# Kernel optimization log

Hardware: AMD Instinct MI355X
Metric: run time of the kernel (lower is better)

Reference implementation:

```python
import jax, jax.numpy as jnp
import numpy as np

B = 256
IN_CH = 1
E = 8          # embedding_channels (power of 2)
DEPTH = 3      # log2(E)
T = 8192       # time_range
WINDOW = 2.0
K = 15         # kernel_size (odd -> torch 'same' == lax 'SAME')
TPI = 2.0 * np.pi


def conv1d(x, w, b, dilation=1, groups=1):
    # x: (B, Cin, T), w: (Cout, Cin/groups, K), b: (Cout,)
    out = jax.lax.conv_general_dilated(
        x, w, window_strides=(1,), padding='SAME',
        rhs_dilation=(dilation,),
        dimension_numbers=('NCH', 'OIH', 'NCH'),
        feature_group_count=groups)
    return out + b[None, :, None]


def setup_inputs() -> dict:
    key = jax.random.key(0)
    ks = jax.random.split(key, 14)
    s = 0.05
    x = jax.random.normal(ks[0], (B, T), jnp.float32)
    W1 = jax.random.normal(ks[1], (E, 2, 1, K), jnp.float32) * s   # per-channel Conv1d(1,2)
    b1 = jax.random.normal(ks[2], (E, 2), jnp.float32) * s
    W2 = jax.random.normal(ks[3], (E, 1, 2, K), jnp.float32) * s   # per-channel Conv1d(2,1)
    b2 = jax.random.normal(ks[4], (E, 1), jnp.float32) * s
    fcW = jax.random.normal(ks[5], (E, 2, T), jnp.float32) * 0.01  # per-channel Linear(T, 2)
    fcb = jax.random.normal(ks[6], (E, 2), jnp.float32) * s
    # deconv tree: level j has 2**(DEPTH-1-j) Conv1d(2,1) units, stacked as grouped conv
    dW0 = jax.random.normal(ks[7], (4, 2, K), jnp.float32) * s
    db0 = jax.random.normal(ks[8], (4,), jnp.float32) * s
    dW1 = jax.random.normal(ks[9], (2, 2, K), jnp.float32) * s
    db1 = jax.random.normal(ks[10], (2,), jnp.float32) * s
    dW2 = jax.random.normal(ks[11], (1, 2, K), jnp.float32) * s
    db2 = jax.random.normal(ks[12], (1,), jnp.float32) * s
    return dict(x=x, W1=W1, b1=b1, W2=W2, b2=b2, fcW=fcW, fcb=fcb,
                dW0=dW0, db0=db0, dW1=dW1, db1=db1, dW2=dW2, db2=db2)


def reference(x, W1, b1, W2, b2, fcW, fcb, dW0, db0, dW1, db1, dW2, db2):
    y = x.reshape(x.shape[0], IN_CH, T)
    # per-channel dilated conv stack (dilation = 2**i)
    chans = []
    for i in range(E):
        h = conv1d(y, W1[i], b1[i], dilation=2 ** i)
        chans.append(conv1d(h, W2[i], b2[i], dilation=2 ** i))
    latent = jnp.concatenate(chans, axis=1)                # (B, E, T)
    # FFT -> frequency / amplitude / offset
    rfft = jnp.fft.rfft(latent, axis=2)                    # (B, E, T//2+1)
    power = jnp.abs(rfft[:, :, 1:]) ** 2
    freqs = jnp.asarray(np.fft.rfftfreq(T)[1:] * T / WINDOW, jnp.float32)
    psum = jnp.sum(power, axis=2)
    f = jnp.sum(freqs * power, axis=2) / psum              # (B, E)
    a = 2.0 * jnp.sqrt(psum) / T
    b_off = rfft.real[:, :, 0] / T
    # per-channel Linear(T, 2) -> phase
    v = jnp.einsum('bet,ect->bec', latent, fcW) + fcb      # (B, E, 2)
    p = jnp.arctan2(v[..., 1], v[..., 0]) / TPI            # (B, E)
    # sinusoid reconstruction
    args = jnp.linspace(-WINDOW / 2, WINDOW / 2, T, dtype=jnp.float32)
    sig = a[..., None] * jnp.sin(TPI * (f[..., None] * args + p[..., None])) + b_off[..., None]
    # deconv tree: pairs of channels -> grouped conv, halving channels each level
    y = sig
    for dW, db in ((dW0, db0), (dW1, db1), (dW2, db2)):
        y = conv1d(y, dW, db, dilation=1, groups=dW.shape[0])
    out = y.reshape(y.shape[0], IN_CH * T)
    return (out, latent, sig,
            p[..., None], f[..., None], a[..., None], b_off[..., None])
```

## Files before the change

kernel.cpp:

```cpp
#include <hip/hip_runtime.h>
#include <math.h>

#define TT 8192
#define BB 256
#define EE 8
#define KK 15
#define PI_F  3.14159265358979323846f
#define TPI_F 6.28318530717958647692f

#define OFF_OUT 0
#define OFF_LAT (BB*TT)
#define OFF_SIG (OFF_LAT + BB*EE*TT)
#define OFF_P   (OFF_SIG + BB*EE*TT)
#define OFF_F   (OFF_P + BB*EE)
#define OFF_A   (OFF_F + BB*EE)
#define OFF_B0  (OFF_A + BB*EE)

#define TILE_C 1024

#define SWZ(i) ((i) + ((i) >> 5))

__global__ __launch_bounds__(512) void conv_stack_kernel(
    const float* __restrict__ x, const float* __restrict__ W1,
    const float* __restrict__ b1, const float* __restrict__ W2,
    const float* __restrict__ b2, float* __restrict__ latent)
{
  extern __shared__ float smem[];
  const int e = blockIdx.x, b = blockIdx.y;
  const int d  = 1 << e;
  const int M  = TT >> e;
  const int Lp = ((((M - 2) + 31) >> 5) << 5) + 30;
  float* sxp = smem;
  float* sW  = smem + d * Lp;
  const int tid = threadIdx.x;
  const float* xr = x + b * TT;

  const int nstage = TT + 28 * d;
  for (int i = tid; i < nstage; i += 512) {
    int t  = i - 14 * d;
    int ph = i & (d - 1);
    int n  = i >> e;
    sxp[ph * Lp + n] = (t >= 0 && t < TT) ? xr[t] : 0.0f;
  }

  if (tid < 29) {
    float acc = 0.0f;
    for (int c = 0; c < 2; c++) {
      const float* w1 = W1 + e*30 + c*15;
      const float* w2 = W2 + e*30 + c*15;
      int jlo = tid - 14; if (jlo < 0) jlo = 0;
      int jhi = tid;      if (jhi > 14) jhi = 14;
      for (int j = jlo; j <= jhi; j++) acc += w2[j] * w1[tid - j];
    }
    sW[tid] = acc;
  } else if (tid == 29) {
    float s20 = 0.f, s21 = 0.f;
    for (int j = 0; j < 15; j++) { s20 += W2[e*30 + j]; s21 += W2[e*30 + 15 + j]; }
    sW[29] = b2[e] + s20*b1[e*2] + s21*b1[e*2 + 1];
  } else if (tid >= 32 && tid < 62) {
    sW[tid] = W1[e*30 + (tid - 32)];
  } else if (tid >= 64 && tid < 94) {
    sW[tid] = W2[e*30 + (tid - 64)];
  } else if (tid == 94 || tid == 95) {
    sW[tid] = b1[e*2 + (tid - 94)];
  }
  __syncthreads();

  float W[29];
  #pragma unroll
  for (int s = 0; s < 29; s++) W[s] = sW[s];
  const float Bc = sW[29];

  float* lr = latent + (b * EE + e) * TT;
  #pragma unroll 1
  for (int g = 0; g < 4; g++) {
    const int vt = g * 512 + tid;
    const int ph = vt & (d - 1);
    const int m0 = (vt >> e) << 2;
    const int row = ph * Lp;

    float win[32];
    {
      const float2* wp = (const float2*)&sxp[row + m0];
      #pragma unroll
      for (int v = 0; v < 16; v++) {
        float2 qv = wp[v];
        win[2*v] = qv.x; win[2*v+1] = qv.y;
      }
    }
    float acc[4] = {Bc, Bc, Bc, Bc};
    #pragma unroll
    for (int s = 0; s < 29; s++) {
      #pragma unroll
      for (int r = 0; r < 4; r++) acc[r] = fmaf(W[s], win[s + r], acc[r]);
    }

    if (g == 0 && m0 <= 6) {
      float h0[10], h1[10];
      #pragma unroll
      for (int s = 0; s < 10; s++) {
        float a0 = sW[94], a1 = sW[95];
        #pragma unroll
        for (int k = 0; k < 15; k++) {
          float xv = win[s + k];
          a0 = fmaf(sW[32 + k], xv, a0);
          a1 = fmaf(sW[47 + k], xv, a1);
        }
        h0[s] = a0; h1[s] = a1;
      }
      #pragma unroll
      for (int r = 0; r < 4; r++) {
        float corr = 0.0f;
        #pragma unroll
        for (int j = 0; j < 7; j++) {
          if (m0 + r + j <= 6) {
            corr = fmaf(sW[64 + j], h0[r + j], corr);
            corr = fmaf(sW[79 + j], h1[r + j], corr);
          }
        }
        acc[r] -= corr;
      }
    }
    if (g == 3 && m0 + 3 >= M - 7) {
      float h0[10], h1[10];
      #pragma unroll
      for (int s = 0; s < 10; s++) {
        float a0 = sW[94], a1 = sW[95];
        #pragma unroll
        for (int k = 0; k < 15; k++) {
          float xv = win[8 + s + k];
          a0 = fmaf(sW[32 + k], xv, a0);
          a1 = fmaf(sW[47 + k], xv, a1);
        }
        h0[s] = a0; h1[s] = a1;
      }
      #pragma unroll
      for (int r = 0; r < 4; r++) {
        float corr = 0.0f;
        #pragma unroll
        for (int jj = 0; jj < 7; jj++) {
          const int j = 8 + jj;
          if (m0 + r + j >= M + 7) {
            corr = fmaf(sW[64 + j], h0[r + jj], corr);
            corr = fmaf(sW[79 + j], h1[r + jj], corr);
          }
        }
        acc[r] -= corr;
      }
    }

    #pragma unroll
    for (int r = 0; r < 4; r++) lr[ph + (m0 + r) * d] = acc[r];
  }
}

#define NF 4096

__device__ __forceinline__ int rev4(int k) {
  unsigned r = __brev((unsigned)k) >> 20;
  return (int)(((r & 0x555u) << 1) | ((r >> 1) & 0x555u));
}

__global__ __launch_bounds__(512) void fft_kernel(
    const float* __restrict__ latent, const float* __restrict__ fcW,
    const float* __restrict__ fcb, float* __restrict__ outP,
    float* __restrict__ outF, float* __restrict__ outA, float* __restrict__ outB0)
{
  __shared__ float re[SWZ(NF - 1) + 1];
  __shared__ float im[SWZ(NF - 1) + 1];
  __shared__ float rbuf[32];
  const int e = blockIdx.x, b = blockIdx.y, tid = threadIdx.x;
  const float2* row2 = (const float2*)(latent + (b*EE + e)*TT);
  const float2* f02  = (const float2*)(fcW + (e*2 + 0)*TT);
  const float2* f12  = (const float2*)(fcW + (e*2 + 1)*TT);

  float v0 = 0.f, v1 = 0.f;
  for (int n = tid; n < NF; n += 512) {
    float2 z = row2[n];
    re[SWZ(n)] = z.x; im[SWZ(n)] = z.y;
    float2 a0 = f02[n], a1 = f12[n];
    v0 = fmaf(z.x, a0.x, v0); v0 = fmaf(z.y, a0.y, v0);
    v1 = fmaf(z.x, a1.x, v1); v1 = fmaf(z.y, a1.y, v1);
  }
  __syncthreads();

  for (int L = NF >> 2; L >= 1; L >>= 2) {
    float wstep = -1.57079632679f / (float)L;
    for (int u = tid; u < (NF >> 2); u += 512) {
      int p = u & (L - 1);
      int base = ((u - p) << 2) + p;
      int i0 = SWZ(base), i1 = SWZ(base + L), i2 = SWZ(base + 2*L), i3 = SWZ(base + 3*L);
      float ar = re[i0], ai = im[i0];
      float br = re[i1], bi = im[i1];
      float cr = re[i2], ci = im[i2];
      float dr = re[i3], di = im[i3];
      float t0r = ar + cr, t0i = ai + ci;
      float t1r = ar - cr, t1i = ai - ci;
      float t2r = br + dr, t2i = bi + di;
      float t3r = br - dr, t3i = bi - di;
      float A0r = t0r + t2r, A0i = t0i + t2i;
      float A1r = t1r + t3i, A1i = t1i - t3r;
      float A2r = t0r - t2r, A2i = t0i - t2i;
      float A3r = t1r - t3i, A3i = t1i + t3r;
      float ang = wstep * (float)p;
      float s1 = __sinf(ang), c1 = __cosf(ang);
      float c2 = c1*c1 - s1*s1, s2 = 2.f*c1*s1;
      float c3 = c1*c2 - s1*s2, s3 = c1*s2 + s1*c2;
      re[i0] = A0r;                 im[i0] = A0i;
      re[i1] = A1r*c1 - A1i*s1;     im[i1] = A1r*s1 + A1i*c1;
      re[i2] = A2r*c2 - A2i*s2;     im[i2] = A2r*s2 + A2i*c2;
      re[i3] = A3r*c3 - A3i*s3;     im[i3] = A3r*s3 + A3i*c3;
    }
    __syncthreads();
  }

  float pacc = 0.f, facc = 0.f;
  for (int k = 1 + tid; k < NF; k += 512) {
    int jk = SWZ(rev4(k));
    int jm = SWZ(rev4(NF - k));
    float zr = re[jk], zi = im[jk];
    float yr = re[jm], yi = im[jm];
    float Er = 0.5f*(zr + yr), Ei = 0.5f*(zi - yi);
    float Dr = 0.5f*(zr - yr), Di = 0.5f*(zi + yi);
    float Or = Di, Oi = -Dr;
    float ang = -PI_F * (float)k / (float)NF;
    float s = __sinf(ang), c = __cosf(ang);
    float Xr = Er + c*Or - s*Oi;
    float Xi = Ei + c*Oi + s*Or;
    float mag = fmaf(Xr, Xr, Xi*Xi);
    pacc += mag;
    facc = fmaf(0.5f * (float)k, mag, facc);
  }
  if (tid == 0) {
    float X = re[SWZ(0)] - im[SWZ(0)];
    pacc += X*X;
    facc += 2048.0f * X*X;
  }

  #pragma unroll
  for (int off = 32; off > 0; off >>= 1) {
    pacc += __shfl_down(pacc, off);
    facc += __shfl_down(facc, off);
    v0   += __shfl_down(v0, off);
    v1   += __shfl_down(v1, off);
  }
  int wid = tid >> 6, lane = tid & 63;
  if (lane == 0) {
    rbuf[wid*4 + 0] = pacc; rbuf[wid*4 + 1] = facc;
    rbuf[wid*4 + 2] = v0;   rbuf[wid*4 + 3] = v1;
  }
  __syncthreads();
  if (tid == 0) {
    float P = 0.f, Fw = 0.f, V0 = 0.f, V1 = 0.f;
    #pragma unroll
    for (int w = 0; w < 8; w++) {
      P += rbuf[w*4]; Fw += rbuf[w*4+1]; V0 += rbuf[w*4+2]; V1 += rbuf[w*4+3];
    }
    float z0r = re[SWZ(0)], z0i = im[SWZ(0)];
    float amp  = 2.0f * sqrtf(P) / (float)TT;
    float boff = (z0r + z0i) / (float)TT;
    float vv0 = V0 + fcb[e*2 + 0];
    float vv1 = V1 + fcb[e*2 + 1];
    float ph  = atan2f(vv1, vv0) / TPI_F;
    int idx = b*EE + e;
    outP[idx]  = ph;
    outF[idx]  = Fw / P;
    outA[idx]  = amp;
    outB0[idx] = boff;
  }
}

#define SST 1068
#define SL0 1056
#define SL1 1040

__global__ __launch_bounds__(256) void sig_deconv_kernel(
    const float* __restrict__ Pv, const float* __restrict__ Fv,
    const float* __restrict__ Av, const float* __restrict__ B0v,
    const float* __restrict__ dW0, const float* __restrict__ db0,
    const float* __restrict__ dW1, const float* __restrict__ db1,
    const float* __restrict__ dW2, const float* __restrict__ db2,
    float* __restrict__ sig, float* __restrict__ out)
{
  __shared__ float smem[4*SL0 + 8*SST];
  float* sl0  = smem;
  float* ssig = smem + 4*SL0;
  float* sl1  = smem + 4*SL0;

  const int tile = blockIdx.x, b = blockIdx.y;
  const int t0 = tile * TILE_C;
  const int tid = threadIdx.x;
  const float step = 2.0f / 8191.0f;

  float fs[8], am[8], psh[8], bo[8];
  #pragma unroll
  for (int ch = 0; ch < EE; ch++) {
    int idx = b*EE + ch;
    fs[ch] = Fv[idx]; am[ch] = Av[idx]; psh[ch] = Pv[idx]; bo[ch] = B0v[idx];
  }

  for (int i = tid; i < SST; i += 256) {
    int t = t0 + i - 21;
    bool in = (i < 1066 && t >= 0 && t < TT);
    float arg = fmaf(step, (float)t, -1.0f);
    bool wr = (i >= 21 && i < 21 + TILE_C);
    #pragma unroll
    for (int ch = 0; ch < EE; ch++) {
      float rr = fmaf(fs[ch], arg, psh[ch]);
      rr -= rintf(rr);
      float val = in ? fmaf(am[ch], __sinf(TPI_F * rr), bo[ch]) : 0.0f;
      ssig[ch*SST + i] = val;
      if (wr) sig[(b*EE + ch)*TT + t] = val;
    }
  }
  __syncthreads();

  for (int g = 0; g < 4; g++) {
    float bg = db0[g];
    for (int u = tid; u < 263; u += 256) {
      const float4* p0 = (const float4*)(ssig + (2*g)*SST + 4*u);
      const float4* p1 = (const float4*)(ssig + (2*g+1)*SST + 4*u);
      float w0[20], w1[20];
      #pragma unroll
      for (int v = 0; v < 5; v++) {
        float4 q0 = p0[v], q1 = p1[v];
        w0[4*v]=q0.x; w0[4*v+1]=q0.y; w0[4*v+2]=q0.z; w0[4*v+3]=q0.w;
        w1[4*v]=q1.x; w1[4*v+1]=q1.y; w1[4*v+2]=q1.z; w1[4*v+3]=q1.w;
      }
      #pragma unroll
      for (int r = 0; r < 4; r++) {
        int i0 = 4*u + r;
        int t = t0 + i0 - 14;
        float a2 = bg;
        #pragma unroll
        for (int k = 0; k < KK; k++) {
          a2 = fmaf(dW0[g*30 + k],      w0[r + k], a2);
          a2 = fmaf(dW0[g*30 + 15 + k], w1[r + k], a2);
        }
        sl0[g*SL0 + i0] = (t >= 0 && t < TT) ? a2 : 0.0f;
      }
    }
  }
  if (tid < 16) sl0[(tid >> 2)*SL0 + 1052 + (tid & 3)] = 0.0f;
  __syncthreads();

  for (int g = 0; g < 2; g++) {
    float bg = db1[g];
    for (int u = tid; u < 260; u += 256) {
      const float4* p0 = (const float4*)(sl0 + (2*g)*SL0 + 4*u);
      const float4* p1 = (const float4*)(sl0 + (2*g+1)*SL0 + 4*u);
      float w0[20], w1[20];
      #pragma unroll
      for (int v = 0; v < 5; v++) {
        float4 q0 = p0[v], q1 = p1[v];
        w0[4*v]=q0.x; w0[4*v+1]=q0.y; w0[4*v+2]=q0.z; w0[4*v+3]=q0.w;
        w1[4*v]=q1.x; w1[4*v+1]=q1.y; w1[4*v+2]=q1.z; w1[4*v+3]=q1.w;
      }
      #pragma unroll
      for (int r = 0; r < 4; r++) {
        int i1 = 4*u + r;
        if (i1 < 1038) {
          int t = t0 + i1 - 7;
          float a2 = bg;
          #pragma unroll
          for (int k = 0; k < KK; k++) {
            a2 = fmaf(dW1[g*30 + k],      w0[r + k], a2);
            a2 = fmaf(dW1[g*30 + 15 + k], w1[r + k], a2);
          }
          sl1[g*SL1 + i1] = (t >= 0 && t < TT) ? a2 : 0.0f;
        }
      }
    }
  }
  __syncthreads();

  {
    float bg = db2[0];
    float* orow = out + b*TT + t0;
    int u = tid;
    const float4* p0 = (const float4*)(sl1 + 4*u);
    const float4* p1 = (const float4*)(sl1 + SL1 + 4*u);
    float w0[20], w1[20];
    #pragma unroll
    for (int v = 0; v < 5; v++) {
      float4 q0 = p0[v], q1 = p1[v];
      w0[4*v]=q0.x; w0[4*v+1]=q0.y; w0[4*v+2]=q0.z; w0[4*v+3]=q0.w;
      w1[4*v]=q1.x; w1[4*v+1]=q1.y; w1[4*v+2]=q1.z; w1[4*v+3]=q1.w;
    }
    float4 res;
    float* resf = (float*)&res;
    #pragma unroll
    for (int r = 0; r < 4; r++) {
      float a2 = bg;
      #pragma unroll
      for (int k = 0; k < KK; k++) {
        a2 = fmaf(dW2[k],      w0[r + k], a2);
        a2 = fmaf(dW2[15 + k], w1[r + k], a2);
      }
      resf[r] = a2;
    }
    ((float4*)orow)[u] = res;
  }
}

extern "C" void kernel_launch(void* const* d_in, const int* in_sizes, int n_in,
                              void* d_out, int out_size, void* d_ws, size_t ws_size,
                              hipStream_t stream) {
  const float* x   = (const float*)d_in[0];
  const float* W1  = (const float*)d_in[1];
  const float* b1  = (const float*)d_in[2];
  const float* W2  = (const float*)d_in[3];
  const float* b2  = (const float*)d_in[4];
  const float* fcW = (const float*)d_in[5];
  const float* fcb = (const float*)d_in[6];
  const float* dW0 = (const float*)d_in[7];
  const float* db0 = (const float*)d_in[8];
  const float* dW1 = (const float*)d_in[9];
  const float* db1 = (const float*)d_in[10];
  const float* dW2 = (const float*)d_in[11];
  const float* db2 = (const float*)d_in[12];

  float* o        = (float*)d_out;
  float* out_main = o + OFF_OUT;
  float* latent   = o + OFF_LAT;
  float* sig      = o + OFF_SIG;
  float* pP  = o + OFF_P;
  float* pF  = o + OFF_F;
  float* pA  = o + OFF_A;
  float* pB0 = o + OFF_B0;

  const size_t lds_conv = 12128 * sizeof(float);
  conv_stack_kernel<<<dim3(EE, BB), 512, lds_conv, stream>>>(x, W1, b1, W2, b2, latent);
  fft_kernel<<<dim3(EE, BB), 512, 0, stream>>>(latent, fcW, fcb, pP, pF, pA, pB0);
  sig_deconv_kernel<<<dim3(TT/TILE_C, BB), 256, 0, stream>>>(
      pP, pF, pA, pB0, dW0, db0, dW1, db1, dW2, db2, sig, out_main);
}
```

Baseline: 353.2 us.

## Split conv stack into time halves and shrink deconv tiles

The conv stack kernel now splits each (batch, channel) row into two time halves across a third grid dimension, staging only half the input plus halo into LDS. This lowers LDS use per block and doubles the block count. The edge-correction code is restructured to recompute the intermediate values inline rather than holding h0/h1 arrays, which should lower register pressure. Weights are broadcast with readfirstlane so they can live in scalar registers. The sig/deconv kernel tile shrinks from 1024 to 512, giving more blocks but more halo recomputation, and half the threads sit idle in the final stage.

```diff
diff --git a/kernel.cpp b/kernel.cpp
--- a/kernel.cpp
+++ b/kernel.cpp
@@ -16,9 +16,11 @@
 #define OFF_A   (OFF_F + BB*EE)
 #define OFF_B0  (OFF_A + BB*EE)
 
-#define TILE_C 1024
-
 #define SWZ(i) ((i) + ((i) >> 5))
+
+__device__ __forceinline__ float rdfl(float v) {
+  return __uint_as_float(__builtin_amdgcn_readfirstlane(__float_as_uint(v)));
+}
 
 __global__ __launch_bounds__(512) void conv_stack_kernel(
     const float* __restrict__ x, const float* __restrict__ W1,
@@ -26,18 +28,20 @@
     const float* __restrict__ b2, float* __restrict__ latent)
 {
   extern __shared__ float smem[];
-  const int e = blockIdx.x, b = blockIdx.y;
+  const int h = blockIdx.x;
+  const int e = blockIdx.y, b = blockIdx.z;
   const int d  = 1 << e;
-  const int M  = TT >> e;
-  const int Lp = ((((M - 2) + 31) >> 5) << 5) + 30;
+  const int Mh = (TT/2) >> e;
+  const int Lp = ((((Mh - 2) + 31) >> 5) << 5) + 30;
   float* sxp = smem;
   float* sW  = smem + d * Lp;
   const int tid = threadIdx.x;
   const float* xr = x + b * TT;
-
-  const int nstage = TT + 28 * d;
+  const int tbase = h * (TT/2) - 14 * d;
+
+  const int nstage = (TT/2) + 28 * d;
   for (int i = tid; i < nstage; i += 512) {
-    int t  = i - 14 * d;
+    int t  = tbase + i;
     int ph = i & (d - 1);
     int n  = i >> e;
     sxp[ph * Lp + n] = (t >= 0 && t < TT) ? xr[t] : 0.0f;
@@ -66,22 +70,21 @@
   }
   __syncthreads();
 
-  float W[29];
+  float Wc[29];
   #pragma unroll
-  for (int s = 0; s < 29; s++) W[s] = sW[s];
-  const float Bc = sW[29];
-
-  float* lr = latent + (b * EE + e) * TT;
+  for (int s = 0; s < 29; s++) Wc[s] = rdfl(sW[s]);
+  const float Bc = rdfl(sW[29]);
+
+  float* lr = latent + (b * EE + e) * TT + h * (TT/2);
   #pragma unroll 1
-  for (int g = 0; g < 4; g++) {
+  for (int g = 0; g < 2; g++) {
     const int vt = g * 512 + tid;
     const int ph = vt & (d - 1);
     const int m0 = (vt >> e) << 2;
-    const int row = ph * Lp;
 
     float win[32];
     {
-      const float2* wp = (const float2*)&sxp[row + m0];
+      const float2* wp = (const float2*)&sxp[ph * Lp + m0];
       #pragma unroll
       for (int v = 0; v < 16; v++) {
         float2 qv = wp[v];
@@ -92,57 +95,47 @@
     #pragma unroll
     for (int s = 0; s < 29; s++) {
       #pragma unroll
-      for (int r = 0; r < 4; r++) acc[r] = fmaf(W[s], win[s + r], acc[r]);
-    }
-
-    if (g == 0 && m0 <= 6) {
-      float h0[10], h1[10];
-      #pragma unroll
-      for (int s = 0; s < 10; s++) {
-        float a0 = sW[94], a1 = sW[95];
-        #pragma unroll
-        for (int k = 0; k < 15; k++) {
-          float xv = win[s + k];
-          a0 = fmaf(sW[32 + k], xv, a0);
-          a1 = fmaf(sW[47 + k], xv, a1);
-        }
-        h0[s] = a0; h1[s] = a1;
-      }
+      for (int r = 0; r < 4; r++) acc[r] = fmaf(Wc[s], win[s + r], acc[r]);
+    }
+
+    if (h == 0 && g == 0 && m0 <= 6) {
       #pragma unroll
       for (int r = 0; r < 4; r++) {
         float corr = 0.0f;
         #pragma unroll
         for (int j = 0; j < 7; j++) {
           if (m0 + r + j <= 6) {
-            corr = fmaf(sW[64 + j], h0[r + j], corr);
-            corr = fmaf(sW[79 + j], h1[r + j], corr);
+            float a0 = sW[94], a1 = sW[95];
+            #pragma unroll
+            for (int k = 0; k < 15; k++) {
+              float xv = win[r + j + k];
+              a0 = fmaf(sW[32 + k], xv, a0);
+              a1 = fmaf(sW[47 + k], xv, a1);
+            }
+            corr = fmaf(sW[64 + j], a0, corr);
+            corr = fmaf(sW[79 + j], a1, corr);
           }
         }
         acc[r] -= corr;
       }
     }
-    if (g == 3 && m0 + 3 >= M - 7) {
-      float h0[10], h1[10];
-      #pragma unroll
-      for (int s = 0; s < 10; s++) {
-        float a0 = sW[94], a1 = sW[95];
-        #pragma unroll
-        for (int k = 0; k < 15; k++) {
-          float xv = win[8 + s + k];
-          a0 = fmaf(sW[32 + k], xv, a0);
-          a1 = fmaf(sW[47 + k], xv, a1);
-        }
-        h0[s] = a0; h1[s] = a1;
-      }
+    if (h == 1 && g == 1 && m0 + 3 >= Mh - 7) {
       #pragma unroll
       for (int r = 0; r < 4; r++) {
         float corr = 0.0f;
         #pragma unroll
         for (int jj = 0; jj < 7; jj++) {
           const int j = 8 + jj;
-          if (m0 + r + j >= M + 7) {
-            corr = fmaf(sW[64 + j], h0[r + jj], corr);
-            corr = fmaf(sW[79 + j], h1[r + jj], corr);
+          if (m0 + r + j >= Mh + 7) {
+            float a0 = sW[94], a1 = sW[95];
+            #pragma unroll
+            for (int k = 0; k < 15; k++) {
+              float xv = win[r + j + k];
+              a0 = fmaf(sW[32 + k], xv, a0);
+              a1 = fmaf(sW[47 + k], xv, a1);
+            }
+            corr = fmaf(sW[64 + j], a0, corr);
+            corr = fmaf(sW[79 + j], a1, corr);
           }
         }
         acc[r] -= corr;
@@ -270,9 +263,10 @@
   }
 }
 
-#define SST 1068
-#define SL0 1056
-#define SL1 1040
+#define TILE_C 512
+#define SST 556
+#define SL0 544
+#define SL1 528
 
 __global__ __launch_bounds__(256) void sig_deconv_kernel(
     const float* __restrict__ Pv, const float* __restrict__ Fv,
@@ -301,7 +295,7 @@
 
   for (int i = tid; i < SST; i += 256) {
     int t = t0 + i - 21;
-    bool in = (i < 1066 && t >= 0 && t < TT);
+    bool in = (i < 554 && t >= 0 && t < TT);
     float arg = fmaf(step, (float)t, -1.0f);
     bool wr = (i >= 21 && i < 21 + TILE_C);
     #pragma unroll
@@ -317,7 +311,7 @@
 
   for (int g = 0; g < 4; g++) {
     float bg = db0[g];
-    for (int u = tid; u < 263; u += 256) {
+    for (int u = tid; u < 135; u += 256) {
       const float4* p0 = (const float4*)(ssig + (2*g)*SST + 4*u);
       const float4* p1 = (const float4*)(ssig + (2*g+1)*SST + 4*u);
       float w0[20], w1[20];
@@ -341,12 +335,12 @@
       }
     }
   }
-  if (tid < 16) sl0[(tid >> 2)*SL0 + 1052 + (tid & 3)] = 0.0f;
+  if (tid < 16) sl0[(tid >> 2)*SL0 + 540 + (tid & 3)] = 0.0f;
   __syncthreads();
 
   for (int g = 0; g < 2; g++) {
     float bg = db1[g];
-    for (int u = tid; u < 260; u += 256) {
+    for (int u = tid; u < 132; u += 256) {
       const float4* p0 = (const float4*)(sl0 + (2*g)*SL0 + 4*u);
       const float4* p1 = (const float4*)(sl0 + (2*g+1)*SL0 + 4*u);
       float w0[20], w1[20];
@@ -359,7 +353,7 @@
       #pragma unroll
       for (int r = 0; r < 4; r++) {
         int i1 = 4*u + r;
-        if (i1 < 1038) {
+        if (i1 < 526) {
           int t = t0 + i1 - 7;
           float a2 = bg;
           #pragma unroll
@@ -374,7 +368,7 @@
   }
   __syncthreads();
 
-  {
+  if (tid < 128) {
     float bg = db2[0];
     float* orow = out + b*TT + t0;
     int u = tid;
@@ -429,8 +423,8 @@
   float* pA  = o + OFF_A;
   float* pB0 = o + OFF_B0;
 
-  const size_t lds_conv = 12128 * sizeof(float);
-  conv_stack_kernel<<<dim3(EE, BB), 512, lds_conv, stream>>>(x, W1, b1, W2, b2, latent);
+  const size_t lds_conv = 8032 * sizeof(float);
+  conv_stack_kernel<<<dim3(2, EE, BB), 512, lds_conv, stream>>>(x, W1, b1, W2, b2, latent);
   fft_kernel<<<dim3(EE, BB), 512, 0, stream>>>(latent, fcW, fcb, pP, pF, pA, pB0);
   sig_deconv_kernel<<<dim3(TT/TILE_C, BB), 256, 0, stream>>>(
       pP, pF, pA, pB0, dW0, db0, dW1, db1, dW2, db2, sig, out_main);
```

Result: no change. 349.4 us (-1.1%).
